# Kernel tuning notes

Hardware: AMD Instinct MI355X
Metric: run time of the kernel (lower is better)

Reference implementation:

```python
import jax, jax.numpy as jnp
import numpy as np

B, D, F = 32768, 512, 512  # batch, input features, output features (num_feats)


def setup_inputs() -> dict:
    key = jax.random.key(0)
    kx, kw, ka, kb = jax.random.split(key, 4)
    x = jax.random.normal(kx, (B, D), dtype=jnp.float32)
    W = jax.random.normal(kw, (F, D), dtype=jnp.float32) / np.float32(np.sqrt(D))
    a = jax.random.normal(ka, (F,), dtype=jnp.float32)
    b = jax.random.normal(kb, (F,), dtype=jnp.float32)
    return {"x": x, "W": W, "a": a, "b": b}


def reference(x, W, a, b):
    # Vectorized form of the nested map_fn:
    # out[i, f] = tanh(b[f] + a[f] * dot(W[f, :], x[i, :]))
    z = jnp.einsum('bd,fd->bf', x, W)  # [B, F] GEMM replacing per-(sample,feature) dots
    return jnp.tanh(a * z + b)
```

## Files before the change

### kernel.cpp

```cpp
#include <hip/hip_runtime.h>
#include <hip/hip_bf16.h>
#include <math.h>


typedef short     bf16x8 __attribute__((ext_vector_type(8)));
typedef float     f32x4  __attribute__((ext_vector_type(4)));
typedef unsigned short u16x4 __attribute__((ext_vector_type(4)));

static constexpr int Mdim = 32768;
static constexpr int Kdim = 512;
static constexpr int Ndim = 512;

__device__ __forceinline__ void split_store(unsigned short* __restrict__ hiP,
                                            unsigned short* __restrict__ loP,
                                            int row, int col4, f32x4 v) {
  u16x4 hi, lo;
#pragma unroll
  for (int j = 0; j < 4; ++j) {
    unsigned bbits = __float_as_uint(v[j]);
    hi[j] = (unsigned short)(bbits >> 16);
    float hf = __uint_as_float(bbits & 0xFFFF0000u);
    float lf = v[j] - hf;
    lo[j] = (unsigned short)(__float_as_uint(lf) >> 16);
  }
  const int k    = col4 * 4;
  const int slot = k >> 3;
  const int off  = row * 64 + ((slot ^ (row & 7)) << 3) + (k & 7);
  *(u16x4*)(hiP + off) = hi;
  *(u16x4*)(loP + off) = lo;
}

__global__ __launch_bounds__(256, 2) void gemm_split_tanh(
    const float* __restrict__ X, const float* __restrict__ Wm,
    const float* __restrict__ avec, const float* __restrict__ bvec,
    float* __restrict__ out) {
  __shared__ unsigned short lds[4][128 * 64];

  const int bid = blockIdx.x;
  const int nB  = bid & 3;
  const int mB  = bid >> 2;
  const int tid  = threadIdx.x;
  const int lane = tid & 63;
  const int wid  = tid >> 6;
  const int wm = wid >> 1, wn = wid & 1;

  f32x4 acc[4][4];
#pragma unroll
  for (int i = 0; i < 4; ++i)
#pragma unroll
    for (int j = 0; j < 4; ++j) acc[i][j] = {0.f, 0.f, 0.f, 0.f};

  const int srow  = tid >> 4;
  const int scol4 = tid & 15;
  const float* Xb = X  + (size_t)mB * 128 * Kdim;
  const float* Wb = Wm + (size_t)nB * 128 * Kdim;

  for (int kt = 0; kt < Kdim / 64; ++kt) {
    const int kbase = kt * 64;
#pragma unroll
    for (int i = 0; i < 8; ++i) {
      const int row = srow + i * 16;
      f32x4 va = *(const f32x4*)(Xb + (size_t)row * Kdim + kbase + scol4 * 4);
      f32x4 vb = *(const f32x4*)(Wb + (size_t)row * Kdim + kbase + scol4 * 4);
      split_store(lds[0], lds[1], row, scol4, va);
      split_store(lds[2], lds[3], row, scol4, vb);
    }
    __syncthreads();

#pragma unroll
    for (int ks = 0; ks < 2; ++ks) {
      bf16x8 ah[4], al[4], bh[4], bl[4];
      const int slotBase = ks * 4 + (lane >> 4);
#pragma unroll
      for (int mi = 0; mi < 4; ++mi) {
        const int row = wm * 64 + mi * 16 + (lane & 15);
        const int off = row * 64 + ((slotBase ^ (row & 7)) << 3);
        ah[mi] = *(const bf16x8*)&lds[0][off];
        al[mi] = *(const bf16x8*)&lds[1][off];
      }
#pragma unroll
      for (int ni = 0; ni < 4; ++ni) {
        const int row = wn * 64 + ni * 16 + (lane & 15);
        const int off = row * 64 + ((slotBase ^ (row & 7)) << 3);
        bh[ni] = *(const bf16x8*)&lds[2][off];
        bl[ni] = *(const bf16x8*)&lds[3][off];
      }
#pragma unroll
      for (int mi = 0; mi < 4; ++mi)
#pragma unroll
        for (int ni = 0; ni < 4; ++ni) {
          acc[mi][ni] = __builtin_amdgcn_mfma_f32_16x16x32_bf16(ah[mi], bh[ni], acc[mi][ni], 0, 0, 0);
          acc[mi][ni] = __builtin_amdgcn_mfma_f32_16x16x32_bf16(ah[mi], bl[ni], acc[mi][ni], 0, 0, 0);
          acc[mi][ni] = __builtin_amdgcn_mfma_f32_16x16x32_bf16(al[mi], bh[ni], acc[mi][ni], 0, 0, 0);
        }
    }
    __syncthreads();
  }

  const int c  = lane & 15;
  const int rq = (lane >> 4) * 4;
#pragma unroll
  for (int ni = 0; ni < 4; ++ni) {
    const int gc = nB * 128 + wn * 64 + ni * 16 + c;
    const float aa = avec[gc];
    const float bb = bvec[gc];
#pragma unroll
    for (int mi = 0; mi < 4; ++mi) {
      const int gr = mB * 128 + wm * 64 + mi * 16 + rq;
      f32x4 v = acc[mi][ni];
#pragma unroll
      for (int j = 0; j < 4; ++j) {
        out[(size_t)(gr + j) * Ndim + gc] = tanhf(aa * v[j] + bb);
      }
    }
  }
}

extern "C" void kernel_launch(void* const* d_in, const int* in_sizes, int n_in,
                              void* d_out, int out_size, void* d_ws, size_t ws_size,
                              hipStream_t stream) {
  const float* X  = (const float*)d_in[0];
  const float* Wm = (const float*)d_in[1];
  const float* av = (const float*)d_in[2];
  const float* bv = (const float*)d_in[3];
  float* out = (float*)d_out;
  dim3 grid((Mdim / 128) * (Ndim / 128));
  dim3 block(256);
  gemm_split_tanh<<<grid, block, 0, stream>>>(X, Wm, av, bv, out);
}
```

Baseline: 177.5 us.

## Prefetch next K tile into registers, use 512 threads, packed bf16 split, fast tanh

The kernel now loads the next K-slice of X and W into registers while the current slice runs through the MFMAs, overlapping global loads with compute. Block size doubles to 512 threads (8 waves, each doing a 64x32 tile), so more waves per CU hide latency. The hi/lo bf16 split uses the packed v_cvt_pk_bf16_f32 instruction, and tanhf is replaced by an exp/rcp approximation. These add register pressure and change rounding: the hi part now rounds instead of truncating, and the fast tanh is less accurate than tanhf.

```diff
diff --git a/kernel.cpp b/kernel.cpp
--- a/kernel.cpp
+++ b/kernel.cpp
@@ -3,34 +3,38 @@
 #include <math.h>
 
 
-typedef short     bf16x8 __attribute__((ext_vector_type(8)));
-typedef float     f32x4  __attribute__((ext_vector_type(4)));
-typedef unsigned short u16x4 __attribute__((ext_vector_type(4)));
+typedef short        bf16x8 __attribute__((ext_vector_type(8)));
+typedef float        f32x4  __attribute__((ext_vector_type(4)));
+typedef unsigned int u32x2  __attribute__((ext_vector_type(2)));
 
 static constexpr int Mdim = 32768;
 static constexpr int Kdim = 512;
 static constexpr int Ndim = 512;
 
-__device__ __forceinline__ void split_store(unsigned short* __restrict__ hiP,
-                                            unsigned short* __restrict__ loP,
-                                            int row, int col4, f32x4 v) {
-  u16x4 hi, lo;
-#pragma unroll
-  for (int j = 0; j < 4; ++j) {
-    unsigned bbits = __float_as_uint(v[j]);
-    hi[j] = (unsigned short)(bbits >> 16);
-    float hf = __uint_as_float(bbits & 0xFFFF0000u);
-    float lf = v[j] - hf;
-    lo[j] = (unsigned short)(__float_as_uint(lf) >> 16);
-  }
-  const int k    = col4 * 4;
-  const int slot = k >> 3;
-  const int off  = row * 64 + ((slot ^ (row & 7)) << 3) + (k & 7);
-  *(u16x4*)(hiP + off) = hi;
-  *(u16x4*)(loP + off) = lo;
+__device__ __forceinline__ unsigned cvt_pk_bf16(float a, float b) {
+  unsigned r;
+  asm("v_cvt_pk_bf16_f32 %0, %1, %2" : "=v"(r) : "v"(a), "v"(b));
+  return r;
 }
 
-__global__ __launch_bounds__(256, 2) void gemm_split_tanh(
+__device__ __forceinline__ void split4(f32x4 v, u32x2& hi, u32x2& lo) {
+  unsigned h0 = cvt_pk_bf16(v[0], v[1]);
+  unsigned h1 = cvt_pk_bf16(v[2], v[3]);
+  float f0 = __uint_as_float(h0 << 16);
+  float f1 = __uint_as_float(h0 & 0xFFFF0000u);
+  float f2 = __uint_as_float(h1 << 16);
+  float f3 = __uint_as_float(h1 & 0xFFFF0000u);
+  lo[0] = cvt_pk_bf16(v[0] - f0, v[1] - f1);
+  lo[1] = cvt_pk_bf16(v[2] - f2, v[3] - f3);
+  hi[0] = h0; hi[1] = h1;
+}
+
+__device__ __forceinline__ float fast_tanh(float x) {
+  float e = __expf(2.0f * x);
+  return 1.0f - 2.0f * __builtin_amdgcn_rcpf(e + 1.0f);
+}
+
+__global__ __launch_bounds__(512, 4) void gemm_split_tanh(
     const float* __restrict__ X, const float* __restrict__ Wm,
     const float* __restrict__ avec, const float* __restrict__ bvec,
     float* __restrict__ out) {
@@ -42,57 +46,78 @@
   const int tid  = threadIdx.x;
   const int lane = tid & 63;
   const int wid  = tid >> 6;
-  const int wm = wid >> 1, wn = wid & 1;
+  const int wm = wid >> 2, wn = wid & 3;
 
-  f32x4 acc[4][4];
+  f32x4 acc[4][2];
 #pragma unroll
   for (int i = 0; i < 4; ++i)
 #pragma unroll
-    for (int j = 0; j < 4; ++j) acc[i][j] = {0.f, 0.f, 0.f, 0.f};
+    for (int j = 0; j < 2; ++j) acc[i][j] = {0.f, 0.f, 0.f, 0.f};
 
   const int srow  = tid >> 4;
   const int scol4 = tid & 15;
+  const int kcol  = scol4 * 4;
+  const int soff0 = ((kcol >> 3)) ;
   const float* Xb = X  + (size_t)mB * 128 * Kdim;
   const float* Wb = Wm + (size_t)nB * 128 * Kdim;
 
+  f32x4 rA[4], rB[4];
+#pragma unroll
+  for (int i = 0; i < 4; ++i) {
+    const int row = srow + 32 * i;
+    rA[i] = *(const f32x4*)(Xb + (size_t)row * Kdim + kcol);
+    rB[i] = *(const f32x4*)(Wb + (size_t)row * Kdim + kcol);
+  }
+
   for (int kt = 0; kt < Kdim / 64; ++kt) {
-    const int kbase = kt * 64;
 #pragma unroll
-    for (int i = 0; i < 8; ++i) {
-      const int row = srow + i * 16;
-      f32x4 va = *(const f32x4*)(Xb + (size_t)row * Kdim + kbase + scol4 * 4);
-      f32x4 vb = *(const f32x4*)(Wb + (size_t)row * Kdim + kbase + scol4 * 4);
-      split_store(lds[0], lds[1], row, scol4, va);
-      split_store(lds[2], lds[3], row, scol4, vb);
+    for (int i = 0; i < 4; ++i) {
+      const int row = srow + 32 * i;
+      const int off = row * 64 + (((soff0) ^ (row & 7)) << 3) + (kcol & 7);
+      u32x2 h, l;
+      split4(rA[i], h, l);
+      *(u32x2*)&lds[0][off] = h;
+      *(u32x2*)&lds[1][off] = l;
+      split4(rB[i], h, l);
+      *(u32x2*)&lds[2][off] = h;
+      *(u32x2*)&lds[3][off] = l;
     }
     __syncthreads();
 
+    if (kt != Kdim / 64 - 1) {
+      const int kbase = (kt + 1) * 64;
+#pragma unroll
+      for (int i = 0; i < 4; ++i) {
+        const int row = srow + 32 * i;
+        rA[i] = *(const f32x4*)(Xb + (size_t)row * Kdim + kbase + kcol);
+        rB[i] = *(const f32x4*)(Wb + (size_t)row * Kdim + kbase + kcol);
+      }
+    }
+
 #pragma unroll
     for (int ks = 0; ks < 2; ++ks) {
-      bf16x8 ah[4], al[4], bh[4], bl[4];
       const int slotBase = ks * 4 + (lane >> 4);
+      bf16x8 bh[2], bl[2];
 #pragma unroll
-      for (int mi = 0; mi < 4; ++mi) {
-        const int row = wm * 64 + mi * 16 + (lane & 15);
-        const int off = row * 64 + ((slotBase ^ (row & 7)) << 3);
-        ah[mi] = *(const bf16x8*)&lds[0][off];
-        al[mi] = *(const bf16x8*)&lds[1][off];
-      }
-#pragma unroll
-      for (int ni = 0; ni < 4; ++ni) {
-        const int row = wn * 64 + ni * 16 + (lane & 15);
+      for (int ni = 0; ni < 2; ++ni) {
+        const int row = wn * 32 + ni * 16 + (lane & 15);
         const int off = row * 64 + ((slotBase ^ (row & 7)) << 3);
         bh[ni] = *(const bf16x8*)&lds[2][off];
         bl[ni] = *(const bf16x8*)&lds[3][off];
       }
 #pragma unroll
-      for (int mi = 0; mi < 4; ++mi)
+      for (int mi = 0; mi < 4; ++mi) {
+        const int row = wm * 64 + mi * 16 + (lane & 15);
+        const int off = row * 64 + ((slotBase ^ (row & 7)) << 3);
+        bf16x8 ah = *(const bf16x8*)&lds[0][off];
+        bf16x8 al = *(const bf16x8*)&lds[1][off];
 #pragma unroll
-        for (int ni = 0; ni < 4; ++ni) {
-          acc[mi][ni] = __builtin_amdgcn_mfma_f32_16x16x32_bf16(ah[mi], bh[ni], acc[mi][ni], 0, 0, 0);
-          acc[mi][ni] = __builtin_amdgcn_mfma_f32_16x16x32_bf16(ah[mi], bl[ni], acc[mi][ni], 0, 0, 0);
-          acc[mi][ni] = __builtin_amdgcn_mfma_f32_16x16x32_bf16(al[mi], bh[ni], acc[mi][ni], 0, 0, 0);
+        for (int ni = 0; ni < 2; ++ni) {
+          acc[mi][ni] = __builtin_amdgcn_mfma_f32_16x16x32_bf16(ah, bh[ni], acc[mi][ni], 0, 0, 0);
+          acc[mi][ni] = __builtin_amdgcn_mfma_f32_16x16x32_bf16(ah, bl[ni], acc[mi][ni], 0, 0, 0);
+          acc[mi][ni] = __builtin_amdgcn_mfma_f32_16x16x32_bf16(al, bh[ni], acc[mi][ni], 0, 0, 0);
         }
+      }
     }
     __syncthreads();
   }
@@ -100,8 +125,8 @@
   const int c  = lane & 15;
   const int rq = (lane >> 4) * 4;
 #pragma unroll
-  for (int ni = 0; ni < 4; ++ni) {
-    const int gc = nB * 128 + wn * 64 + ni * 16 + c;
+  for (int ni = 0; ni < 2; ++ni) {
+    const int gc = nB * 128 + wn * 32 + ni * 16 + c;
     const float aa = avec[gc];
     const float bb = bvec[gc];
 #pragma unroll
@@ -110,7 +135,7 @@
       f32x4 v = acc[mi][ni];
 #pragma unroll
       for (int j = 0; j < 4; ++j) {
-        out[(size_t)(gr + j) * Ndim + gc] = tanhf(aa * v[j] + bb);
+        out[(size_t)(gr + j) * Ndim + gc] = fast_tanh(aa * v[j] + bb);
       }
     }
   }
@@ -125,6 +150,6 @@
   const float* bv = (const float*)d_in[3];
   float* out = (float*)d_out;
   dim3 grid((Mdim / 128) * (Ndim / 128));
-  dim3 block(256);
+  dim3 block(512);
   gemm_split_tanh<<<grid, block, 0, stream>>>(X, Wm, av, bv, out);
 }
```

Result: faster. 157.9 us (-11.0%).
